# Kernel tuning notes

Hardware: AMD Instinct MI355X
Metric: run time of the kernel (lower is better)

## Reference

```python
import jax, jax.numpy as jnp
import numpy as np

N = 50000      # nodes
E = 300000     # edges per relation
IN = 128       # in_feats
HF = 64        # h_feats
AH = 4         # att_heads
R = 3          # relations
H = HF * AH    # 256, per-relation hidden width


def setup_inputs() -> dict:
    key = jax.random.key(0)
    ks = jax.random.split(key, 10)
    s = 0.05
    h = jax.random.normal(ks[0], (N, IN), jnp.float32)
    # relation_aware params (shared across relations)
    dW = jax.random.normal(ks[1], (IN, H), jnp.float32) * s
    db = jnp.zeros((H,), jnp.float32)
    fW = jax.random.normal(ks[2], (3 * H, 1), jnp.float32) * s
    fb = jnp.zeros((1,), jnp.float32)
    # per-relation H2FDLayer params (stacked over R)
    wW = jax.random.normal(ks[3], (R, IN, H), jnp.float32) * s
    wb = jnp.zeros((R, H), jnp.float32)
    aW = jax.random.normal(ks[4], (R, 2 * HF, 1), jnp.float32) * s
    ab = jnp.zeros((R, 1), jnp.float32)
    # final combining linear
    linW = jax.random.normal(ks[5], (R * H, H), jnp.float32) * s
    linb = jnp.zeros((H,), jnp.float32)
    src = jax.random.randint(ks[6], (R, E), 0, N, jnp.int32)
    dst = jax.random.randint(ks[7], (R, E), 0, N, jnp.int32)
    return dict(h=h, dW=dW, db=db, fW=fW, fb=fb, wW=wW, wb=wb,
                aW=aW, ab=ab, linW=linW, linb=linb, src=src, dst=dst)


def _segment_softmax(alpha, seg, num_segments):
    # alpha: [E, AH]; softmax over edges sharing the same destination node
    amax = jax.ops.segment_max(alpha, seg, num_segments=num_segments)
    ex = jnp.exp(alpha - amax[seg])
    denom = jax.ops.segment_sum(ex, seg, num_segments=num_segments)
    return ex / denom[seg]


def reference(h, dW, db, fW, fb, wW, wb, aW, ab, linW, linb, src, dst):
    hd = h @ dW + db  # [N, H] relation_aware d_liner (shared)
    outs = []
    for r in range(R):
        s_idx, d_idx = src[r], dst[r]
        sd, dd = hd[s_idx], hd[d_idx]  # [E, H]
        # sign_edges: tanh(f_liner(cat[src,dst,src-dst])) -> sign
        score = jnp.tanh((jnp.concatenate([sd, dd, sd - dd], axis=1) @ fW + fb)[:, 0])
        sign = jnp.sign(score)  # [E]
        hw = h @ wW[r] + wb[r]  # [N, H] per-relation w_liner
        sf = (sign[:, None] * hw[s_idx]).reshape(E, AH, HF)          # signed src features
        z = jnp.concatenate([sf, hw[d_idx].reshape(E, AH, HF)], -1)  # [E, AH, 2*HF]
        alpha = jax.nn.leaky_relu((z @ aW[r] + ab[r])[..., 0], 0.01)  # [E, AH]
        w = _segment_softmax(alpha, d_idx, N)                         # [E, AH]
        out_r = jax.ops.segment_sum(w[..., None] * sf, d_idx, num_segments=N)
        outs.append(out_r.reshape(N, H))
    out = jnp.concatenate(outs, axis=1)  # [N, R*H]
    return out @ linW + linb             # [N, H]
```

## Files before the change

kernel.cpp:

```cpp
#include <hip/hip_runtime.h>

#define NN 50000
#define MP 50048
#define EE 300000
#define KIN 128
#define HH 256
#define KOUT 768
#define NAH 4
#define NHF 64
#define NR 3

#define GSH 7
#define NG 391
#define NBKT (NR * NG)
#define BCAP 1024
#define EPB 16384
#define NTOT (NR * EE)

typedef __attribute__((ext_vector_type(8))) short short8_t;
typedef __attribute__((ext_vector_type(4))) float f32x4;

#define O_DBL   0ull
#define O_AVEC  2080ull
#define O_ACON  14368ull
#define O_GS    14464ull
#define O_GD    214464ull
#define O_ASRC  414464ull
#define O_ADST  2814464ull
#define O_GCNT  5214464ull
#define O_GBUF  5222656ull
#define O_H16   10027264ull
#define O_WT    22839552ull
#define O_LWT   23036160ull
#define O_HW16  23429376ull
#define O_OUTA  100303104ull

__device__ __forceinline__ ushort f2bf(float x) {
  union { float f; unsigned u; } c; c.f = x;
  return (ushort)((c.u + 0x7FFFu + ((c.u >> 16) & 1u)) >> 16);
}
__device__ __forceinline__ float bf2f(ushort u) {
  return __uint_as_float(((unsigned)u) << 16);
}

__global__ void k_prep(const float* __restrict__ dW, const float* __restrict__ db,
                       const float* __restrict__ fW, const float* __restrict__ wW,
                       const float* __restrict__ wb, const float* __restrict__ aW,
                       double* __restrict__ dbuf, float* __restrict__ avec,
                       float* __restrict__ acon) {
  int b = blockIdx.x, t = threadIdx.x;
  if (b == 0) {
    if (t < KIN) {
      double p = 0.0, q = 0.0;
      for (int j = 0; j < HH; ++j) {
        double u = (double)fW[j] + (double)fW[2 * HH + j];
        double v = (double)fW[HH + j] - (double)fW[2 * HH + j];
        double w = (double)dW[t * HH + j];
        p += w * u; q += w * v;
      }
      dbuf[t] = p; dbuf[KIN + t] = q;
    } else if (t == KIN) {
      double cu = 0.0, cv = 0.0;
      for (int j = 0; j < HH; ++j) {
        double u = (double)fW[j] + (double)fW[2 * HH + j];
        double v = (double)fW[HH + j] - (double)fW[2 * HH + j];
        cu += (double)db[j] * u; cv += (double)db[j] * v;
      }
      dbuf[2 * KIN] = cu; dbuf[2 * KIN + 1] = cv;
    }
  } else if (b <= 12) {
    int idx = (b - 1) * 256 + t;
    int d = idx >> 7, k = idx & 127;
    int r = d >> 3, rem = d & 7, ah = rem >> 1, which = rem & 1;
    const float* wWr = wW + (size_t)r * KIN * HH;
    const float* aWr = aW + (size_t)r * 2 * NHF + which * NHF;
    float s = 0.f;
    for (int f = 0; f < NHF; ++f) s += wWr[(size_t)k * HH + ah * NHF + f] * aWr[f];
    avec[idx] = s;
  } else {
    if (t < 24) {
      int d = t, r = d >> 3, rem = d & 7, ah = rem >> 1, which = rem & 1;
      const float* aWr = aW + (size_t)r * 2 * NHF + which * NHF;
      const float* wbr = wb + (size_t)r * HH + ah * NHF;
      float s = 0.f;
      for (int f = 0; f < NHF; ++f) s += wbr[f] * aWr[f];
      acon[d] = s;
    }
  }
}

__global__ __launch_bounds__(256) void k_fuse(const float* __restrict__ h,
                                              const double* __restrict__ dbuf,
                                              const float* __restrict__ avec,
                                              const float* __restrict__ acon,
                                              float* __restrict__ gs, float* __restrict__ gd,
                                              ushort* __restrict__ h16,
                                              float* __restrict__ asrcAll,
                                              float* __restrict__ adstAll) {
  int bid = blockIdx.x;
  if (bid == NN / 4) {
    for (int i = threadIdx.x; i < (MP - NN) * KIN / 8; i += 256) {
      short8_t z = {0, 0, 0, 0, 0, 0, 0, 0};
      *(short8_t*)&h16[(size_t)NN * KIN + i * 8] = z;
    }
    return;
  }
  int node = (int)((bid * 256u + threadIdx.x) >> 6);
  int lane = threadIdx.x & 63;
  float2 hv = *(const float2*)&h[(size_t)node * KIN + lane * 2];
  ushort2 o2; o2.x = f2bf(hv.x); o2.y = f2bf(hv.y);
  *(ushort2*)&h16[(size_t)node * KIN + lane * 2] = o2;
  double ps = (double)hv.x * dbuf[lane * 2] + (double)hv.y * dbuf[lane * 2 + 1];
  double qs = (double)hv.x * dbuf[KIN + lane * 2] + (double)hv.y * dbuf[KIN + lane * 2 + 1];
#pragma unroll
  for (int m = 32; m; m >>= 1) { ps += __shfl_xor(ps, m, 64); qs += __shfl_xor(qs, m, 64); }
  float res[24];
#pragma unroll
  for (int d = 0; d < 24; ++d) {
    float p = hv.x * avec[d * 128 + 2 * lane] + hv.y * avec[d * 128 + 2 * lane + 1];
#pragma unroll
    for (int m = 32; m; m >>= 1) p += __shfl_xor(p, m, 64);
    res[d] = p;
  }
  if (lane == 0) {
    gs[node] = (float)(ps + dbuf[2 * KIN]);
    gd[node] = (float)(qs + dbuf[2 * KIN + 1]);
#pragma unroll
    for (int r = 0; r < NR; ++r) {
      float4 va, vd;
      va.x = res[r * 8 + 0] + acon[r * 8 + 0]; vd.x = res[r * 8 + 1] + acon[r * 8 + 1];
      va.y = res[r * 8 + 2] + acon[r * 8 + 2]; vd.y = res[r * 8 + 3] + acon[r * 8 + 3];
      va.z = res[r * 8 + 4] + acon[r * 8 + 4]; vd.z = res[r * 8 + 5] + acon[r * 8 + 5];
      va.w = res[r * 8 + 6] + acon[r * 8 + 6]; vd.w = res[r * 8 + 7] + acon[r * 8 + 7];
      *(float4*)&asrcAll[(size_t)r * NN * NAH + (size_t)node * NAH] = va;
      *(float4*)&adstAll[(size_t)r * NN * NAH + (size_t)node * NAH] = vd;
    }
  }
}

#define WT_ELEMS (NR * HH * KIN)
#define LWT_ELEMS (HH * KOUT)
__global__ __launch_bounds__(256) void k_cvtW(const float* __restrict__ wW, const float* __restrict__ linW,
                                              ushort* __restrict__ Wt, ushort* __restrict__ LWt) {
  int t = blockIdx.x * 256 + threadIdx.x;
  if (t < WT_ELEMS) {
    int r = t / (HH * KIN), rem = t % (HH * KIN);
    int n = rem / KIN, k = rem % KIN;
    Wt[t] = f2bf(wW[((size_t)r * KIN + k) * HH + n]);
  }
  int u = t - WT_ELEMS;
  if (u >= 0 && u < LWT_ELEMS) {
    int n = u / KOUT, kk = u % KOUT;
    LWt[u] = f2bf(linW[(size_t)kk * HH + n]);
  }
}

template <int K, bool BIAS, bool OBF16>
__global__ __launch_bounds__(256) void k_mm(const ushort* __restrict__ A0,
                                            const ushort* __restrict__ Bt0,
                                            const float* __restrict__ bias0,
                                            void* __restrict__ Cv, int M, int bStride,
                                            size_t btZ, size_t biasZ, size_t cZ) {
  __shared__ ushort As[128][40];
  __shared__ ushort Bs[128][40];
  const ushort* A = A0;
  const ushort* Bt = Bt0 + (size_t)blockIdx.z * btZ;
  const float* bias = BIAS ? bias0 + (size_t)blockIdx.z * biasZ : bias0;
  size_t cOfs = (size_t)blockIdx.z * cZ;
  int bm = blockIdx.x * 128, bn = blockIdx.y * 128;
  int tid = threadIdx.x, lane = tid & 63, w = tid >> 6;
  int wm = w >> 1, wn = w & 1;
  int sr = tid >> 2, sk = (tid & 3) * 8;
  int fr = lane & 15, kb = (lane >> 4) * 8;
  const bool aok0 = (bm + sr) < M, aok1 = (bm + 64 + sr) < M;
  f32x4 acc[4][4] = {};
  for (int k0 = 0; k0 < K; k0 += 32) {
    short8_t a0 = {0, 0, 0, 0, 0, 0, 0, 0}, a1 = {0, 0, 0, 0, 0, 0, 0, 0};
    if (aok0) a0 = *(const short8_t*)&A[(size_t)(bm + sr) * K + k0 + sk];
    if (aok1) a1 = *(const short8_t*)&A[(size_t)(bm + 64 + sr) * K + k0 + sk];
    short8_t b0 = *(const short8_t*)&Bt[(size_t)(bn + sr) * bStride + k0 + sk];
    short8_t b1 = *(const short8_t*)&Bt[(size_t)(bn + 64 + sr) * bStride + k0 + sk];
    __syncthreads();
    *(short8_t*)&As[sr][sk] = a0;
    *(short8_t*)&As[64 + sr][sk] = a1;
    *(short8_t*)&Bs[sr][sk] = b0;
    *(short8_t*)&Bs[64 + sr][sk] = b1;
    __syncthreads();
    short8_t af[4], bfr[4];
#pragma unroll
    for (int i = 0; i < 4; ++i) af[i] = *(const short8_t*)&As[wm * 64 + i * 16 + fr][kb];
#pragma unroll
    for (int i = 0; i < 4; ++i) bfr[i] = *(const short8_t*)&Bs[wn * 64 + i * 16 + fr][kb];
#pragma unroll
    for (int i = 0; i < 4; ++i)
#pragma unroll
      for (int j = 0; j < 4; ++j)
        acc[i][j] = __builtin_amdgcn_mfma_f32_16x16x32_bf16(af[i], bfr[j], acc[i][j], 0, 0, 0);
  }
  int rq = lane >> 4;
#pragma unroll
  for (int i = 0; i < 4; ++i) {
#pragma unroll
    for (int j = 0; j < 4; ++j) {
      int col = bn + wn * 64 + j * 16 + fr;
      float bv = 0.f;
      if constexpr (BIAS) bv = bias[col];
#pragma unroll
      for (int q = 0; q < 4; ++q) {
        int row = bm + wm * 64 + i * 16 + rq * 4 + q;
        if (row < M) {
          float v = acc[i][j][q] + bv;
          if constexpr (OBF16) ((ushort*)Cv)[cOfs + (size_t)row * HH + col] = f2bf(v);
          else ((float*)Cv)[(size_t)row * HH + col] = v;
        }
      }
    }
  }
}

__global__ __launch_bounds__(512) void k_bin(const int* __restrict__ dst,
                                             int* __restrict__ gcnt,
                                             uint* __restrict__ gbuf) {
  __shared__ int hist[NBKT];
  __shared__ int base[NBKT];
  int tid = threadIdx.x;
  int start = blockIdx.x * EPB;
  for (int b = tid; b < NBKT; b += 512) hist[b] = 0;
  __syncthreads();
#pragma unroll 4
  for (int i = 0; i < EPB / 512; ++i) {
    int e = start + i * 512 + tid;
    if (e < NTOT) {
      int d = dst[e];
      int r = (e >= 2 * EE) ? 2 : ((e >= EE) ? 1 : 0);
      atomicAdd(&hist[r * NG + (d >> GSH)], 1);
    }
  }
  __syncthreads();
  for (int b = tid; b < NBKT; b += 512) {
    int c = hist[b];
    base[b] = (c > 0) ? atomicAdd(&gcnt[b], c) : 0;
    hist[b] = 0;
  }
  __syncthreads();
#pragma unroll 4
  for (int i = 0; i < EPB / 512; ++i) {
    int e = start + i * 512 + tid;
    if (e < NTOT) {
      int d = dst[e];
      int r = (e >= 2 * EE) ? 2 : ((e >= EE) ? 1 : 0);
      int bkt = r * NG + (d >> GSH);
      int idx = base[bkt] + atomicAdd(&hist[bkt], 1);
      if (idx < BCAP)
        gbuf[(size_t)bkt * BCAP + idx] = ((uint)(d & 127) << 19) | (uint)(e - r * EE);
    }
  }
}

__global__ __launch_bounds__(512) void k_edgeB(const int* __restrict__ srcAll,
                                               const ushort* __restrict__ hwAll,
                                               const float* __restrict__ gs,
                                               const float* __restrict__ gd,
                                               const float* __restrict__ asrcAll,
                                               const float* __restrict__ adstAll,
                                               const float* __restrict__ fb,
                                               const float* __restrict__ abAll,
                                               const int* __restrict__ gcnt,
                                               const uint* __restrict__ gbuf,
                                               ushort* __restrict__ out768) {
  __shared__ uint ebuf[BCAP];
  __shared__ uint csr[BCAP];
  __shared__ float gsv[BCAP];
  __shared__ float asv[BCAP * 4];
  __shared__ int cntL[128], offL[128], curL[128];
  int rl = blockIdx.x / NG, g = blockIdx.x % NG;
  const int* src = srcAll + (size_t)rl * EE;
  const ushort* hw = hwAll + (size_t)rl * MP * HH;
  const float* asrc = asrcAll + (size_t)rl * NN * NAH;
  const float* adst = adstAll + (size_t)rl * NN * NAH;
  int tid = threadIdx.x;
  int cb = gcnt[blockIdx.x]; if (cb > BCAP) cb = BCAP;
  if (tid < 128) { cntL[tid] = 0; curL[tid] = 0; }
  __syncthreads();
  for (int i = tid; i < cb; i += 512) {
    uint ent = gbuf[(size_t)blockIdx.x * BCAP + i];
    ebuf[i] = ent;
    atomicAdd(&cntL[ent >> 19], 1);
  }
  __syncthreads();
  if (tid < 64) {
    int c0 = cntL[2 * tid], c1 = cntL[2 * tid + 1];
    int s = c0 + c1, inc = s;
#pragma unroll
    for (int o = 1; o < 64; o <<= 1) {
      int v = __shfl_up(inc, o, 64);
      if (tid >= o) inc += v;
    }
    int ex = inc - s;
    offL[2 * tid] = ex;
    offL[2 * tid + 1] = ex + c0;
  }
  __syncthreads();
  for (int i = tid; i < cb; i += 512) {
    uint ent = ebuf[i];
    int b = (int)(ent >> 19);
    int idx = atomicAdd(&curL[b], 1);
    csr[offL[b] + idx] = ent;
  }
  __syncthreads();
  for (int i = tid; i < cb; i += 512) {
    int sv = src[csr[i] & 0x7FFFFu];
    ebuf[i] = (uint)sv;
    gsv[i] = gs[sv];
    *(float4*)&asv[4 * i] = *(const float4*)&asrc[(size_t)sv * NAH];
  }
  __syncthreads();

  int lane = tid & 63, wv = tid >> 6;
  int head = lane >> 4, iE = lane >> 2, cah = lane & 3;
  float fbv = fb[0], abv = abAll[rl];
  size_t colBase = (size_t)rl * HH + lane * 4;
  for (int it = 0; it < 16; ++it) {
    int ln = wv + 8 * it;
    int node = (g << GSH) + ln;
    if (node >= NN) continue;
    int deg = cntL[ln]; deg = deg < 64 ? deg : 64;
    if (deg == 0) {
      ushort4 z = {0, 0, 0, 0};
      *(ushort4*)&out768[(size_t)node * KOUT + colBase] = z;
      continue;
    }
    int bofs = offL[ln];
    float gdn = gd[node];
    float adn = adst[(size_t)node * NAH + cah];
    float den = 0.f;
    float w_[4]; int s_[4];
#pragma unroll
    for (int p = 0; p < 4; ++p) {
      float wgt = 0.f; int sv = 0;
      if (p * 16 < deg) {
        int e = p * 16 + iE;
        float ex = 0.f;
        if (e < deg) {
          int i = bofs + e;
          sv = (int)ebuf[i];
          float t = gsv[i] + gdn + fbv;
          float sg = (t > 0.f) ? 1.f : ((t < 0.f) ? -1.f : 0.f);
          float a = sg * asv[4 * i + cah] + adn + abv;
          a = (a >= 0.f) ? a : 0.01f * a;
          ex = __expf(a);
          wgt = sg * ex;
        }
        float red = ex;
#pragma unroll
        for (int m = 4; m <= 32; m <<= 1) red += __shfl_xor(red, m, 64);
        den += red;
      }
      w_[p] = wgt; s_[p] = sv;
    }
    float rd = 1.f / __shfl(den, head, 64);
    float4 acc = {0, 0, 0, 0};
#pragma unroll
    for (int p = 0; p < 4; ++p) {
      if (p * 16 >= deg) break;
      int lim = deg - p * 16; lim = lim < 16 ? lim : 16;
      int i2 = 0;
      for (; i2 + 3 < lim; i2 += 4) {
        float w0 = __shfl(w_[p], i2 * 4 + head, 64);
        int   v0 = __shfl(s_[p], i2 * 4 + head, 64);
        float w1 = __shfl(w_[p], i2 * 4 + 4 + head, 64);
        int   v1 = __shfl(s_[p], i2 * 4 + 4 + head, 64);
        float w2 = __shfl(w_[p], i2 * 4 + 8 + head, 64);
        int   v2 = __shfl(s_[p], i2 * 4 + 8 + head, 64);
        float w3 = __shfl(w_[p], i2 * 4 + 12 + head, 64);
        int   v3 = __shfl(s_[p], i2 * 4 + 12 + head, 64);
        ushort4 h0 = *(const ushort4*)&hw[(size_t)v0 * HH + lane * 4];
        ushort4 h1 = *(const ushort4*)&hw[(size_t)v1 * HH + lane * 4];
        ushort4 h2 = *(const ushort4*)&hw[(size_t)v2 * HH + lane * 4];
        ushort4 h3 = *(const ushort4*)&hw[(size_t)v3 * HH + lane * 4];
        acc.x += w0 * bf2f(h0.x) + w1 * bf2f(h1.x) + w2 * bf2f(h2.x) + w3 * bf2f(h3.x);
        acc.y += w0 * bf2f(h0.y) + w1 * bf2f(h1.y) + w2 * bf2f(h2.y) + w3 * bf2f(h3.y);
        acc.z += w0 * bf2f(h0.z) + w1 * bf2f(h1.z) + w2 * bf2f(h2.z) + w3 * bf2f(h3.z);
        acc.w += w0 * bf2f(h0.w) + w1 * bf2f(h1.w) + w2 * bf2f(h2.w) + w3 * bf2f(h3.w);
      }
      for (; i2 < lim; ++i2) {
        float w0 = __shfl(w_[p], i2 * 4 + head, 64);
        int   v0 = __shfl(s_[p], i2 * 4 + head, 64);
        ushort4 h0 = *(const ushort4*)&hw[(size_t)v0 * HH + lane * 4];
        acc.x += w0 * bf2f(h0.x); acc.y += w0 * bf2f(h0.y);
        acc.z += w0 * bf2f(h0.z); acc.w += w0 * bf2f(h0.w);
      }
    }
    ushort4 o;
    o.x = f2bf(acc.x * rd); o.y = f2bf(acc.y * rd);
    o.z = f2bf(acc.z * rd); o.w = f2bf(acc.w * rd);
    *(ushort4*)&out768[(size_t)node * KOUT + colBase] = o;
  }
}

extern "C" void kernel_launch(void* const* d_in, const int* in_sizes, int n_in,
                              void* d_out, int out_size, void* d_ws, size_t ws_size,
                              hipStream_t stream) {
  const float* h    = (const float*)d_in[0];
  const float* dW   = (const float*)d_in[1];
  const float* db   = (const float*)d_in[2];
  const float* fW   = (const float*)d_in[3];
  const float* fb   = (const float*)d_in[4];
  const float* wW   = (const float*)d_in[5];
  const float* wb   = (const float*)d_in[6];
  const float* aW   = (const float*)d_in[7];
  const float* ab   = (const float*)d_in[8];
  const float* linW = (const float*)d_in[9];
  const float* linb = (const float*)d_in[10];
  const int*   src  = (const int*)d_in[11];
  const int*   dst  = (const int*)d_in[12];
  float* out = (float*)d_out;
  char* ws = (char*)d_ws;

  double* dbuf  = (double*)(ws + O_DBL);
  float* avec   = (float*)(ws + O_AVEC);
  float* acon   = (float*)(ws + O_ACON);
  float* gs     = (float*)(ws + O_GS);
  float* gd     = (float*)(ws + O_GD);
  float* asrc   = (float*)(ws + O_ASRC);
  float* adst   = (float*)(ws + O_ADST);
  int*   gcnt   = (int*)(ws + O_GCNT);
  uint*  gbuf   = (uint*)(ws + O_GBUF);
  ushort* h16   = (ushort*)(ws + O_H16);
  ushort* Wt    = (ushort*)(ws + O_WT);
  ushort* LWt   = (ushort*)(ws + O_LWT);
  ushort* hw16  = (ushort*)(ws + O_HW16);
  ushort* out768 = (ushort*)(ws + O_OUTA);

  hipMemsetAsync(ws + O_GCNT, 0, 8192, stream);
  k_prep<<<14, 256, 0, stream>>>(dW, db, fW, wW, wb, aW, dbuf, avec, acon);
  k_fuse<<<NN / 4 + 1, 256, 0, stream>>>(h, dbuf, avec, acon, gs, gd, h16, asrc, adst);
  k_cvtW<<<(WT_ELEMS + LWT_ELEMS + 255) / 256, 256, 0, stream>>>(wW, linW, Wt, LWt);
  k_bin<<<(NTOT + EPB - 1) / EPB, 512, 0, stream>>>(dst, gcnt, gbuf);

  k_mm<KIN, true, true><<<dim3(MP / 128, 2, 3), 256, 0, stream>>>(
      h16, Wt, wb, hw16, MP, KIN, (size_t)HH * KIN, (size_t)HH, (size_t)MP * HH);
  k_edgeB<<<NBKT, 512, 0, stream>>>(
      src, hw16, gs, gd, asrc, adst, fb, ab, gcnt, gbuf, out768);
  k_mm<KOUT, true, false><<<dim3(MP / 128, 2, 1), 256, 0, stream>>>(
      out768, LWt, linb, out, NN, KOUT, 0, 0, 0);
}
```

Before: 424.9 us.

## Compute attention projections from bf16 hw and pack src ids into bin entries

Attention logits are no longer computed in k_fuse by folding aW into wW. A new k_aproj kernel now computes them from the bf16 hw output after the first GEMM, which removes 24 shuffle reductions per node from k_fuse. k_bin now stores the source node index directly in each bucket entry, so k_edgeB no longer does an indirect load from src, and the per-edge source attention scores are staged in LDS as bf16 to cut shared memory. The extra kernel rereads the whole hw tensor (about 77MB), and the bf16 rounding of hw and of the staged scores changes numerics slightly.

```diff
diff --git a/kernel.cpp b/kernel.cpp
--- a/kernel.cpp
+++ b/kernel.cpp
@@ -21,19 +21,17 @@
 typedef __attribute__((ext_vector_type(4))) float f32x4;
 
 #define O_DBL   0ull
-#define O_AVEC  2080ull
-#define O_ACON  14368ull
-#define O_GS    14464ull
-#define O_GD    214464ull
-#define O_ASRC  414464ull
-#define O_ADST  2814464ull
-#define O_GCNT  5214464ull
-#define O_GBUF  5222656ull
-#define O_H16   10027264ull
-#define O_WT    22839552ull
-#define O_LWT   23036160ull
-#define O_HW16  23429376ull
-#define O_OUTA  100303104ull
+#define O_GS    2080ull
+#define O_GD    202080ull
+#define O_ASRC  402080ull
+#define O_ADST  2802080ull
+#define O_GCNT  5202080ull
+#define O_GBUF  5210272ull
+#define O_H16   10014880ull
+#define O_WT    22827168ull
+#define O_LWT   23023776ull
+#define O_HW16  23416992ull
+#define O_OUTA  100290720ull
 
 __device__ __forceinline__ ushort f2bf(float x) {
   union { float f; unsigned u; } c; c.f = x;
@@ -44,59 +42,32 @@
 }
 
 __global__ void k_prep(const float* __restrict__ dW, const float* __restrict__ db,
-                       const float* __restrict__ fW, const float* __restrict__ wW,
-                       const float* __restrict__ wb, const float* __restrict__ aW,
-                       double* __restrict__ dbuf, float* __restrict__ avec,
-                       float* __restrict__ acon) {
-  int b = blockIdx.x, t = threadIdx.x;
-  if (b == 0) {
-    if (t < KIN) {
-      double p = 0.0, q = 0.0;
-      for (int j = 0; j < HH; ++j) {
-        double u = (double)fW[j] + (double)fW[2 * HH + j];
-        double v = (double)fW[HH + j] - (double)fW[2 * HH + j];
-        double w = (double)dW[t * HH + j];
-        p += w * u; q += w * v;
-      }
-      dbuf[t] = p; dbuf[KIN + t] = q;
-    } else if (t == KIN) {
-      double cu = 0.0, cv = 0.0;
-      for (int j = 0; j < HH; ++j) {
-        double u = (double)fW[j] + (double)fW[2 * HH + j];
-        double v = (double)fW[HH + j] - (double)fW[2 * HH + j];
-        cu += (double)db[j] * u; cv += (double)db[j] * v;
-      }
-      dbuf[2 * KIN] = cu; dbuf[2 * KIN + 1] = cv;
-    }
-  } else if (b <= 12) {
-    int idx = (b - 1) * 256 + t;
-    int d = idx >> 7, k = idx & 127;
-    int r = d >> 3, rem = d & 7, ah = rem >> 1, which = rem & 1;
-    const float* wWr = wW + (size_t)r * KIN * HH;
-    const float* aWr = aW + (size_t)r * 2 * NHF + which * NHF;
-    float s = 0.f;
-    for (int f = 0; f < NHF; ++f) s += wWr[(size_t)k * HH + ah * NHF + f] * aWr[f];
-    avec[idx] = s;
-  } else {
-    if (t < 24) {
-      int d = t, r = d >> 3, rem = d & 7, ah = rem >> 1, which = rem & 1;
-      const float* aWr = aW + (size_t)r * 2 * NHF + which * NHF;
-      const float* wbr = wb + (size_t)r * HH + ah * NHF;
-      float s = 0.f;
-      for (int f = 0; f < NHF; ++f) s += wbr[f] * aWr[f];
-      acon[d] = s;
-    }
+                       const float* __restrict__ fW, double* __restrict__ dbuf) {
+  int t = threadIdx.x;
+  if (t < KIN) {
+    double p = 0.0, q = 0.0;
+    for (int j = 0; j < HH; ++j) {
+      double u = (double)fW[j] + (double)fW[2 * HH + j];
+      double v = (double)fW[HH + j] - (double)fW[2 * HH + j];
+      double w = (double)dW[t * HH + j];
+      p += w * u; q += w * v;
+    }
+    dbuf[t] = p; dbuf[KIN + t] = q;
+  } else if (t == KIN) {
+    double cu = 0.0, cv = 0.0;
+    for (int j = 0; j < HH; ++j) {
+      double u = (double)fW[j] + (double)fW[2 * HH + j];
+      double v = (double)fW[HH + j] - (double)fW[2 * HH + j];
+      cu += (double)db[j] * u; cv += (double)db[j] * v;
+    }
+    dbuf[2 * KIN] = cu; dbuf[2 * KIN + 1] = cv;
   }
 }
 
 __global__ __launch_bounds__(256) void k_fuse(const float* __restrict__ h,
                                               const double* __restrict__ dbuf,
-                                              const float* __restrict__ avec,
-                                              const float* __restrict__ acon,
                                               float* __restrict__ gs, float* __restrict__ gd,
-                                              ushort* __restrict__ h16,
-                                              float* __restrict__ asrcAll,
-                                              float* __restrict__ adstAll) {
+                                              ushort* __restrict__ h16) {
   int bid = blockIdx.x;
   if (bid == NN / 4) {
     for (int i = threadIdx.x; i < (MP - NN) * KIN / 8; i += 256) {
@@ -114,27 +85,9 @@
   double qs = (double)hv.x * dbuf[KIN + lane * 2] + (double)hv.y * dbuf[KIN + lane * 2 + 1];
 #pragma unroll
   for (int m = 32; m; m >>= 1) { ps += __shfl_xor(ps, m, 64); qs += __shfl_xor(qs, m, 64); }
-  float res[24];
-#pragma unroll
-  for (int d = 0; d < 24; ++d) {
-    float p = hv.x * avec[d * 128 + 2 * lane] + hv.y * avec[d * 128 + 2 * lane + 1];
-#pragma unroll
-    for (int m = 32; m; m >>= 1) p += __shfl_xor(p, m, 64);
-    res[d] = p;
-  }
   if (lane == 0) {
     gs[node] = (float)(ps + dbuf[2 * KIN]);
     gd[node] = (float)(qs + dbuf[2 * KIN + 1]);
-#pragma unroll
-    for (int r = 0; r < NR; ++r) {
-      float4 va, vd;
-      va.x = res[r * 8 + 0] + acon[r * 8 + 0]; vd.x = res[r * 8 + 1] + acon[r * 8 + 1];
-      va.y = res[r * 8 + 2] + acon[r * 8 + 2]; vd.y = res[r * 8 + 3] + acon[r * 8 + 3];
-      va.z = res[r * 8 + 4] + acon[r * 8 + 4]; vd.z = res[r * 8 + 5] + acon[r * 8 + 5];
-      va.w = res[r * 8 + 6] + acon[r * 8 + 6]; vd.w = res[r * 8 + 7] + acon[r * 8 + 7];
-      *(float4*)&asrcAll[(size_t)r * NN * NAH + (size_t)node * NAH] = va;
-      *(float4*)&adstAll[(size_t)r * NN * NAH + (size_t)node * NAH] = vd;
-    }
   }
 }
 
@@ -218,7 +171,33 @@
   }
 }
 
+__global__ __launch_bounds__(256) void k_aproj(const ushort* __restrict__ hwAll,
+                                               const float* __restrict__ aWAll,
+                                               float* __restrict__ asrcAll,
+                                               float* __restrict__ adstAll) {
+  int r = blockIdx.y;
+  const ushort* hw = hwAll + (size_t)r * MP * HH;
+  const float* aW = aWAll + (size_t)r * 2 * NHF;
+  int node = (int)((blockIdx.x * 256u + threadIdx.x) >> 6);
+  int lane = threadIdx.x & 63;
+  if (node >= NN) return;
+  int ah = lane >> 4, j = lane & 15;
+  ushort4 hv4 = *(const ushort4*)&hw[(size_t)node * HH + ah * NHF + j * 4];
+  float hx = bf2f(hv4.x), hy = bf2f(hv4.y), hz = bf2f(hv4.z), hwv = bf2f(hv4.w);
+  float4 a1 = *(const float4*)&aW[j * 4];
+  float4 a2 = *(const float4*)&aW[NHF + j * 4];
+  float s1 = hx * a1.x + hy * a1.y + hz * a1.z + hwv * a1.w;
+  float s2 = hx * a2.x + hy * a2.y + hz * a2.z + hwv * a2.w;
+#pragma unroll
+  for (int m = 8; m; m >>= 1) { s1 += __shfl_xor(s1, m, 64); s2 += __shfl_xor(s2, m, 64); }
+  if (j == 0) {
+    asrcAll[(size_t)r * NN * NAH + (size_t)node * NAH + ah] = s1;
+    adstAll[(size_t)r * NN * NAH + (size_t)node * NAH + ah] = s2;
+  }
+}
+
 __global__ __launch_bounds__(512) void k_bin(const int* __restrict__ dst,
+                                             const int* __restrict__ src,
                                              int* __restrict__ gcnt,
                                              uint* __restrict__ gbuf) {
   __shared__ int hist[NBKT];
@@ -248,17 +227,17 @@
     int e = start + i * 512 + tid;
     if (e < NTOT) {
       int d = dst[e];
+      int sv = src[e];
       int r = (e >= 2 * EE) ? 2 : ((e >= EE) ? 1 : 0);
       int bkt = r * NG + (d >> GSH);
       int idx = base[bkt] + atomicAdd(&hist[bkt], 1);
       if (idx < BCAP)
-        gbuf[(size_t)bkt * BCAP + idx] = ((uint)(d & 127) << 19) | (uint)(e - r * EE);
-    }
-  }
-}
-
-__global__ __launch_bounds__(512) void k_edgeB(const int* __restrict__ srcAll,
-                                               const ushort* __restrict__ hwAll,
+        gbuf[(size_t)bkt * BCAP + idx] = ((uint)(d & 127) << 17) | (uint)sv;
+    }
+  }
+}
+
+__global__ __launch_bounds__(512) void k_edgeB(const ushort* __restrict__ hwAll,
                                                const float* __restrict__ gs,
                                                const float* __restrict__ gd,
                                                const float* __restrict__ asrcAll,
@@ -271,10 +250,9 @@
   __shared__ uint ebuf[BCAP];
   __shared__ uint csr[BCAP];
   __shared__ float gsv[BCAP];
-  __shared__ float asv[BCAP * 4];
+  __shared__ ushort asv[BCAP * 4];
   __shared__ int cntL[128], offL[128], curL[128];
   int rl = blockIdx.x / NG, g = blockIdx.x % NG;
-  const int* src = srcAll + (size_t)rl * EE;
   const ushort* hw = hwAll + (size_t)rl * MP * HH;
   const float* asrc = asrcAll + (size_t)rl * NN * NAH;
   const float* adst = adstAll + (size_t)rl * NN * NAH;
@@ -285,7 +263,7 @@
   for (int i = tid; i < cb; i += 512) {
     uint ent = gbuf[(size_t)blockIdx.x * BCAP + i];
     ebuf[i] = ent;
-    atomicAdd(&cntL[ent >> 19], 1);
+    atomicAdd(&cntL[ent >> 17], 1);
   }
   __syncthreads();
   if (tid < 64) {
@@ -303,16 +281,18 @@
   __syncthreads();
   for (int i = tid; i < cb; i += 512) {
     uint ent = ebuf[i];
-    int b = (int)(ent >> 19);
+    int b = (int)(ent >> 17);
     int idx = atomicAdd(&curL[b], 1);
     csr[offL[b] + idx] = ent;
   }
   __syncthreads();
   for (int i = tid; i < cb; i += 512) {
-    int sv = src[csr[i] & 0x7FFFFu];
-    ebuf[i] = (uint)sv;
+    int sv = (int)(csr[i] & 0x1FFFFu);
     gsv[i] = gs[sv];
-    *(float4*)&asv[4 * i] = *(const float4*)&asrc[(size_t)sv * NAH];
+    float4 a4 = *(const float4*)&asrc[(size_t)sv * NAH];
+    ushort4 a16; a16.x = f2bf(a4.x); a16.y = f2bf(a4.y);
+    a16.z = f2bf(a4.z); a16.w = f2bf(a4.w);
+    *(ushort4*)&asv[4 * i] = a16;
   }
   __syncthreads();
 
@@ -343,10 +323,10 @@
         float ex = 0.f;
         if (e < deg) {
           int i = bofs + e;
-          sv = (int)ebuf[i];
+          sv = (int)(csr[i] & 0x1FFFFu);
           float t = gsv[i] + gdn + fbv;
           float sg = (t > 0.f) ? 1.f : ((t < 0.f) ? -1.f : 0.f);
-          float a = sg * asv[4 * i + cah] + adn + abv;
+          float a = sg * bf2f(asv[4 * i + cah]) + adn + abv;
           a = (a >= 0.f) ? a : 0.01f * a;
           ex = __expf(a);
           wgt = sg * ex;
@@ -418,8 +398,6 @@
   char* ws = (char*)d_ws;
 
   double* dbuf  = (double*)(ws + O_DBL);
-  float* avec   = (float*)(ws + O_AVEC);
-  float* acon   = (float*)(ws + O_ACON);
   float* gs     = (float*)(ws + O_GS);
   float* gd     = (float*)(ws + O_GD);
   float* asrc   = (float*)(ws + O_ASRC);
@@ -433,15 +411,16 @@
   ushort* out768 = (ushort*)(ws + O_OUTA);
 
   hipMemsetAsync(ws + O_GCNT, 0, 8192, stream);
-  k_prep<<<14, 256, 0, stream>>>(dW, db, fW, wW, wb, aW, dbuf, avec, acon);
-  k_fuse<<<NN / 4 + 1, 256, 0, stream>>>(h, dbuf, avec, acon, gs, gd, h16, asrc, adst);
+  k_prep<<<1, 256, 0, stream>>>(dW, db, fW, dbuf);
+  k_fuse<<<NN / 4 + 1, 256, 0, stream>>>(h, dbuf, gs, gd, h16);
   k_cvtW<<<(WT_ELEMS + LWT_ELEMS + 255) / 256, 256, 0, stream>>>(wW, linW, Wt, LWt);
-  k_bin<<<(NTOT + EPB - 1) / EPB, 512, 0, stream>>>(dst, gcnt, gbuf);
+  k_bin<<<(NTOT + EPB - 1) / EPB, 512, 0, stream>>>(dst, src, gcnt, gbuf);
 
   k_mm<KIN, true, true><<<dim3(MP / 128, 2, 3), 256, 0, stream>>>(
       h16, Wt, wb, hw16, MP, KIN, (size_t)HH * KIN, (size_t)HH, (size_t)MP * HH);
+  k_aproj<<<dim3(NN / 4, 3), 256, 0, stream>>>(hw16, aW, asrc, adst);
   k_edgeB<<<NBKT, 512, 0, stream>>>(
-      src, hw16, gs, gd, asrc, adst, fb, ab, gcnt, gbuf, out768);
+      hw16, gs, gd, asrc, adst, fb, ab, gcnt, gbuf, out768);
   k_mm<KOUT, true, false><<<dim3(MP / 128, 2, 1), 256, 0, stream>>>(
       out768, LWt, linb, out, NN, KOUT, 0, 0, 0);
 }
```

Result: no change. 416.6 us (-2.0%).
